# Optimization experiments

Measured on AMD Instinct MI355X. Metric: run time of the kernel, lower is better.

The kernel has to match this reference:

```python
import jax, jax.numpy as jnp
import numpy as np

N = 4608      # total nodes (48 graphs x 96 nodes)
B = 48
NPG = 96
D = 512       # vec_dim
XD = 16       # x_dim
E = N * 32    # GAT edges
L = 6         # GAT layers


def _w(k, shape, fan_in):
    return jax.random.normal(k, shape, jnp.float32) * (1.0 / np.sqrt(fan_in))


def setup_inputs() -> dict:
    key = jax.random.key(0)
    ks = jax.random.split(key, 24)
    x = jax.random.normal(ks[0], (N, XD), jnp.float32)
    xyz = jax.random.normal(ks[1], (N, 3), jnp.float32)
    edge_index = jax.random.randint(ks[2], (2, E), 0, N, dtype=jnp.int32)
    ptr = (jnp.arange(B + 1) * NPG).astype(jnp.int32)
    # complete graph with replacement per segment (torch.combinations order: i<=j)
    i, j = np.triu_indices(NPG)
    offs = (np.arange(B) * NPG)[:, None]
    cloud_edge_index = jnp.asarray(
        np.stack([(i[None, :] + offs).reshape(-1), (j[None, :] + offs).reshape(-1)]),
        jnp.int32)
    return {
        'x': x, 'edge_index': edge_index, 'ptr': ptr, 'xyz': xyz,
        'cloud_edge_index': cloud_edge_index,
        'x_proj_w': _w(ks[3], (XD, D), XD), 'x_proj_b': jnp.zeros((D,), jnp.float32),
        'gat_wl': _w(ks[4], (L, D, D), D), 'gat_bl': jnp.zeros((L, D), jnp.float32),
        'gat_wr': _w(ks[5], (L, D, D), D), 'gat_br': jnp.zeros((L, D), jnp.float32),
        'gat_att': _w(ks[6], (L, D), D), 'gat_bias': jnp.zeros((L, D), jnp.float32),
        'gat_ln_g': jnp.ones((L - 1, D), jnp.float32), 'gat_ln_b': jnp.zeros((L - 1, D), jnp.float32),
        'cg_xyz_w': _w(ks[7], (3, D), 3),
        'cg_bn_g': jnp.ones((D,), jnp.float32), 'cg_bn_b': jnp.zeros((D,), jnp.float32),
        'cg_lin1_w': _w(ks[8], (D, D), D), 'cg_lin1_b': jnp.zeros((D,), jnp.float32),
        'cg_ln_g': jnp.ones((D,), jnp.float32), 'cg_ln_b': jnp.zeros((D,), jnp.float32),
        'lin_w': _w(ks[9], (D, D), D), 'lin_b': jnp.zeros((D,), jnp.float32),
        'bn_g': jnp.ones((D,), jnp.float32), 'bn_b': jnp.zeros((D,), jnp.float32),
    }


def _batchnorm(t, g, b):
    mu = t.mean(0)
    v = ((t - mu) ** 2).mean(0)
    return (t - mu) / jnp.sqrt(v + 1e-5) * g + b


def _forward(x, edge_index, cloud_edge_index, x_proj_w, x_proj_b, gat_wl, gat_bl,
             gat_wr, gat_br, gat_att, gat_bias, gat_ln_g, gat_ln_b, cg_xyz_w,
             cg_bn_g, cg_bn_b, cg_lin1_w, cg_lin1_b, cg_ln_g, cg_ln_b,
             lin_w, lin_b, bn_g, bn_b, xyz):
    n = x.shape[0]
    h = x @ x_proj_w + x_proj_b  # [N, D]
    # ---- GATv2 stack (heads=1, self-loops added, eval mode: no dropout) ----
    loops = jnp.arange(n, dtype=edge_index.dtype)
    ei = jnp.concatenate([edge_index, jnp.stack([loops, loops])], axis=1)
    src, dst = ei[0], ei[1]
    xg = h
    for l in range(L):
        xl = xg @ gat_wl[l] + gat_bl[l]
        xr = xg @ gat_wr[l] + gat_br[l]
        e = jax.nn.leaky_relu(xl[src] + xr[dst], 0.2) @ gat_att[l]  # [E+N]
        m = jax.ops.segment_max(e, dst, num_segments=n)
        ew = jnp.exp(e - m[dst])
        den = jax.ops.segment_sum(ew, dst, num_segments=n)
        alpha = ew / den[dst]
        out = jax.ops.segment_sum(alpha[:, None] * xl[src], dst, num_segments=n) + gat_bias[l]
        if l < L - 1:
            # PyG LayerNorm, mode='graph', batch=None: normalize over all elements
            mu = out.mean()
            sd = jnp.sqrt(((out - mu) ** 2).mean())
            out = (out - mu) / (sd + 1e-5) * gat_ln_g[l] + gat_ln_b[l]
            out = jax.nn.relu(out)
        xg = out
    # ---- CloudGraph (complete graph gather-compute-scatter) ----
    a, b = cloud_edge_index[0], cloud_edge_index[1]
    rx = h[a] - h[b]          # [Ec, D]
    rz = xyz[a] - xyz[b]      # [Ec, 3]
    sq = (rz ** 2).sum(-1)
    dist = jnp.where(sq > 0, jnp.sqrt(jnp.where(sq > 0, sq, 1.0)), 0.0)
    w = jnp.exp(-dist)[:, None]
    p1 = jax.ops.segment_sum(jax.nn.relu((w * rx) @ cg_lin1_w + cg_lin1_b), a, num_segments=n)
    mu1 = p1.mean(-1, keepdims=True)
    v1 = ((p1 - mu1) ** 2).mean(-1, keepdims=True)
    ln1 = (p1 - mu1) / jnp.sqrt(v1 + 1e-5) * cg_ln_g + cg_ln_b
    p2 = jax.ops.segment_sum(jax.nn.relu(rz @ cg_xyz_w), a, num_segments=n)
    xc = h + ln1 + _batchnorm(p2, cg_bn_g, cg_bn_b)
    # ---- fuse + final norm ----
    return _batchnorm((h + xg + xc) @ lin_w + lin_b, bn_g, bn_b)


def reference(x, edge_index, ptr, xyz, cloud_edge_index, x_proj_w, x_proj_b,
              gat_wl, gat_bl, gat_wr, gat_br, gat_att, gat_bias, gat_ln_g,
              gat_ln_b, cg_xyz_w, cg_bn_g, cg_bn_b, cg_lin1_w, cg_lin1_b,
              cg_ln_g, cg_ln_b, lin_w, lin_b, bn_g, bn_b):
    return _forward(x, edge_index, cloud_edge_index, x_proj_w, x_proj_b, gat_wl,
                    gat_bl, gat_wr, gat_br, gat_att, gat_bias, gat_ln_g,
                    gat_ln_b, cg_xyz_w, cg_bn_g, cg_bn_b, cg_lin1_w, cg_lin1_b,
                    cg_ln_g, cg_ln_b, lin_w, lin_b, bn_g, bn_b, xyz)
```

## Files before the change

kernel.cpp:

```cpp
#include <hip/hip_runtime.h>
#include <hip/hip_bf16.h>

#define NN 4608
#define BG 48
#define NPG 96
#define DD 512
#define XDIM 16
#define EREAL 147456
#define NLAYER 6
#define NK 262144
#define TRIU 4656

typedef __hip_bfloat16 bf16;
typedef short short8 __attribute__((ext_vector_type(8)));
typedef short shortx4 __attribute__((ext_vector_type(4)));
typedef float f32x4 __attribute__((ext_vector_type(4)));
typedef float f32x2 __attribute__((ext_vector_type(2)));

__device__ __forceinline__ float s2f(short s) {
  return __uint_as_float(((unsigned int)(unsigned short)s) << 16);
}
__device__ __forceinline__ short f2bs(float f) {
  bf16 h = __float2bfloat16(f);
  short s;
  __builtin_memcpy(&s, &h, 2);
  return s;
}
__device__ __forceinline__ void f8x4(unsigned int w, float* o) {
  f32x2 a = __builtin_amdgcn_cvt_pk_f32_fp8(w, false);
  f32x2 b = __builtin_amdgcn_cvt_pk_f32_fp8(w, true);
  o[0] = a[0]; o[1] = a[1]; o[2] = b[0]; o[3] = b[1];
}
__device__ __forceinline__ void bf4(uint2 q, float* o) {
  o[0] = s2f((short)(q.x & 0xffff));
  o[1] = s2f((short)(q.x >> 16));
  o[2] = s2f((short)(q.y & 0xffff));
  o[3] = s2f((short)(q.y >> 16));
}

typedef const __attribute__((address_space(1))) unsigned int ga_u32;
typedef __attribute__((address_space(3))) unsigned int ls_u32;
__device__ __forceinline__ void gl16(const void* g, void* l) {
  __builtin_amdgcn_global_load_lds((ga_u32*)g, (ls_u32*)l, 16, 0, 0);
}

__global__ __launch_bounds__(256) void k_wt(const float* __restrict__ wl,
                                            const float* __restrict__ wr,
                                            const float* __restrict__ cg,
                                            const float* __restrict__ lin,
                                            bf16* __restrict__ Wt,
                                            int* __restrict__ counts,
                                            float* __restrict__ statsAll) {
  if (blockIdx.z == 0) {
    int id = (blockIdx.y * 16 + blockIdx.x) * 256 + threadIdx.x;
    if (id < NN) counts[id] = 0;
    if (id < 5 * 32) statsAll[id] = 0.f;
  }
  __shared__ float tile[32][33];
  int z = blockIdx.z;
  const float* src = (z < 6) ? wl + (size_t)z * NK
                   : (z < 12) ? wr + (size_t)(z - 6) * NK
                   : (z == 12) ? cg : lin;
  bf16* dst = Wt + (size_t)z * NK;
  int c = threadIdx.x & 31;
  int r0 = threadIdx.x >> 5;
  int bx = blockIdx.x * 32, by = blockIdx.y * 32;
#pragma unroll
  for (int i = 0; i < 4; i++) {
    int r = r0 + i * 8;
    tile[r][c] = src[(size_t)(by + r) * 512 + bx + c];
  }
  __syncthreads();
#pragma unroll
  for (int i = 0; i < 4; i++) {
    int r = r0 + i * 8;
    dst[(size_t)(bx + r) * 512 + by + c] = __float2bfloat16(tile[c][r]);
  }
}

__global__ void k_xproj(const float* __restrict__ x, const float* __restrict__ w,
                        const float* __restrict__ b, const int* __restrict__ ei,
                        const float* __restrict__ xyz,
                        bf16* __restrict__ h_bf, int* __restrict__ counts,
                        float* __restrict__ ep) {
  int i = blockIdx.x * blockDim.x + threadIdx.x;
  if (i >= NN * DD) return;
  if (i < EREAL) atomicAdd(&counts[ei[EREAL + i]], 1);
  if (i < NN * NPG) {
    int n = i / NPG, e = i - n * NPG;
    int p = n % NPG;
    if (e < NPG - p) {
      int g = n / NPG;
      int slot = g * TRIU + p * NPG - (p * (p - 1)) / 2 + e;
      int j = n + e;
      float dx = xyz[n * 3] - xyz[j * 3];
      float dy = xyz[n * 3 + 1] - xyz[j * 3 + 1];
      float dz = xyz[n * 3 + 2] - xyz[j * 3 + 2];
      float sq = dx * dx + dy * dy + dz * dz;
      float dist = (sq > 0.f) ? sqrtf(sq) : 0.f;
      float4 v;
      v.x = dx; v.y = dy; v.z = dz; v.w = __expf(-dist);
      *(float4*)&ep[(size_t)slot * 4] = v;
    }
  }
  int n = i >> 9, d = i & 511;
  float acc = b[d];
#pragma unroll
  for (int k = 0; k < XDIM; k++) acc += x[n * XDIM + k] * w[k * DD + d];
  h_bf[i] = __float2bfloat16(acc);
}

__global__ void k_scan(const int* __restrict__ counts, int* offsets, int* cursor) {
  __shared__ int part[256];
  int t = threadIdx.x;
  int base = t * 18;
  int s = 0;
#pragma unroll
  for (int i = 0; i < 18; i++) s += counts[base + i];
  part[t] = s;
  __syncthreads();
  for (int off = 1; off < 256; off <<= 1) {
    int v = part[t];
    int u = (t >= off) ? part[t - off] : 0;
    __syncthreads();
    part[t] = v + u;
    __syncthreads();
  }
  int run = t ? part[t - 1] : 0;
#pragma unroll
  for (int i = 0; i < 18; i++) {
    offsets[base + i] = run;
    cursor[base + i] = run;
    run += counts[base + i];
  }
  if (t == 0) offsets[NN] = EREAL;
}
__global__ void k_scatter(const int* __restrict__ ei, int* cursor, int* ssrc) {
  int e = blockIdx.x * blockDim.x + threadIdx.x;
  if (e < EREAL) {
    int s = ei[e], d = ei[EREAL + e];
    int pos = atomicAdd(&cursor[d], 1);
    ssrc[pos] = s;
  }
}

__global__ __launch_bounds__(256) void k_ln(bf16* __restrict__ xg,
                                            const float* __restrict__ stats,
                                            const float* __restrict__ g,
                                            const float* __restrict__ b,
                                            const float* __restrict__ p2,
                                            float* __restrict__ colsum,
                                            float* __restrict__ colsq) {
  if ((int)blockIdx.x >= 1152) {
    int r0 = (blockIdx.x - 1152) * 32;
    int c0 = threadIdx.x;
    float s0 = 0.f, q0 = 0.f, s1 = 0.f, q1 = 0.f;
    for (int r = r0; r < r0 + 32; ++r) {
      float v = p2[(size_t)r * 512 + c0];
      s0 += v; q0 += v * v;
      float w = p2[(size_t)r * 512 + c0 + 256];
      s1 += w; q1 += w * w;
    }
    atomicAdd(&colsum[c0], s0);
    atomicAdd(&colsq[c0], q0);
    atomicAdd(&colsum[c0 + 256], s1);
    atomicAdd(&colsq[c0 + 256], q1);
    return;
  }
  float s = 0.f, ss = 0.f;
#pragma unroll
  for (int i = 0; i < 16; i++) { s += stats[i]; ss += stats[16 + i]; }
  const float invM = 1.f / ((float)NN * (float)DD);
  float mu = s * invM;
  float var = ss * invM - mu * mu;
  float sd = sqrtf(fmaxf(var, 0.f));
  float inv = 1.f / (sd + 1e-5f);
  int i = blockIdx.x * 256 + threadIdx.x;
  int base = i * 8;
  int d0 = base & 511;
  short8 raw = *(const short8*)&xg[base];
  short8 pk;
#pragma unroll
  for (int k = 0; k < 8; k++) {
    float t = fmaxf((s2f(raw[k]) - mu) * inv * g[d0 + k] + b[d0 + k], 0.f);
    pk[k] = f2bs(t);
  }
  *(short8*)&xg[base] = pk;
}

__device__ __forceinline__ void gemm_tile(
    const bf16* __restrict__ Abf, const bf16* __restrict__ B,
    const float* __restrict__ bias,
    float* __restrict__ C, bf16* __restrict__ Cb, unsigned char* __restrict__ Cf8,
    float* __restrict__ csum, float* __restrict__ csq,
    int m0, int n0, bf16* As, bf16* Bs, float* cs, float* cq) {
  int tid = threadIdx.x;
  int lane = tid & 63, wid = tid >> 6;
  int mh = (wid >> 1) * 64, nh = (wid & 1) * 32;
  int l15 = lane & 15, quad = lane >> 4;
  int lr8 = lane >> 3, ls8 = lane & 7;
  int c16l = ls8 ^ lr8;
  int swzr = (l15 & 7) * 8;

  if (csum && tid < 64) { cs[tid] = 0.f; cq[tid] = 0.f; }

  const bf16* aSrc = Abf + (size_t)(m0 + wid * 32 + lr8) * 512 + c16l * 8;
  const bf16* bSrc = B   + (size_t)(n0 + wid * 16 + lr8) * 512 + c16l * 8;

#define STAGE(bi, kt) do {                                                   \
    gl16(aSrc + (kt) * 64,            As + (bi) * 8192 + (wid * 32     ) * 64); \
    gl16(aSrc + (kt) * 64 +  8 * 512, As + (bi) * 8192 + (wid * 32 +  8) * 64); \
    gl16(aSrc + (kt) * 64 + 16 * 512, As + (bi) * 8192 + (wid * 32 + 16) * 64); \
    gl16(aSrc + (kt) * 64 + 24 * 512, As + (bi) * 8192 + (wid * 32 + 24) * 64); \
    gl16(bSrc + (kt) * 64,            Bs + (bi) * 4096 + (wid * 16     ) * 64); \
    gl16(bSrc + (kt) * 64 +  8 * 512, Bs + (bi) * 4096 + (wid * 16 +  8) * 64); \
  } while (0)

  f32x4 acc[4][2];
#pragma unroll
  for (int mt = 0; mt < 4; mt++)
#pragma unroll
    for (int nt = 0; nt < 2; nt++) acc[mt][nt] = (f32x4)0.f;

  STAGE(0, 0);
  __syncthreads();

#pragma unroll
  for (int kt = 0; kt < 8; kt++) {
    const int cur = kt & 1;
    if (kt < 7) STAGE(cur ^ 1, kt + 1);
    short8 af[2][4], bfr[2][2];
#pragma unroll
    for (int kk = 0; kk < 2; kk++) {
#pragma unroll
      for (int mt = 0; mt < 4; mt++)
        af[kk][mt] = *(const short8*)&As[cur * 8192 + (mh + mt * 16 + l15) * 64 +
                                        (((kk * 4 + quad) * 8) ^ swzr)];
#pragma unroll
      for (int nt = 0; nt < 2; nt++)
        bfr[kk][nt] = *(const short8*)&Bs[cur * 4096 + (nh + nt * 16 + l15) * 64 +
                                         (((kk * 4 + quad) * 8) ^ swzr)];
    }
#pragma unroll
    for (int kk = 0; kk < 2; kk++)
#pragma unroll
      for (int mt = 0; mt < 4; mt++)
#pragma unroll
        for (int nt = 0; nt < 2; nt++)
          acc[mt][nt] = __builtin_amdgcn_mfma_f32_16x16x32_bf16(
              bfr[kk][nt], af[kk][mt], acc[mt][nt], 0, 0, 0);
    __syncthreads();
  }
#undef STAGE

  float colS[2][4] = {{0.f,0.f,0.f,0.f},{0.f,0.f,0.f,0.f}};
  float colQ[2][4] = {{0.f,0.f,0.f,0.f},{0.f,0.f,0.f,0.f}};
  float bv[2][4] = {{0.f,0.f,0.f,0.f},{0.f,0.f,0.f,0.f}};
#pragma unroll
  for (int nt = 0; nt < 2; nt++) {
    if (bias) {
      float4 b4 = *(const float4*)&bias[n0 + nh + nt * 16 + quad * 4];
      bv[nt][0] = b4.x; bv[nt][1] = b4.y; bv[nt][2] = b4.z; bv[nt][3] = b4.w;
    }
  }
#pragma unroll
  for (int mt = 0; mt < 4; mt++) {
    int row = m0 + mh + mt * 16 + l15;
#pragma unroll
    for (int nt = 0; nt < 2; nt++) {
      int col0 = n0 + nh + nt * 16 + quad * 4;
      float v[4];
#pragma unroll
      for (int r2 = 0; r2 < 4; r2++) {
        v[r2] = acc[mt][nt][r2] + bv[nt][r2];
        if (csum) { colS[nt][r2] += v[r2]; colQ[nt][r2] += v[r2] * v[r2]; }
      }
      if (C) {
        float4 o; o.x = v[0]; o.y = v[1]; o.z = v[2]; o.w = v[3];
        *(float4*)&C[(size_t)row * 512 + col0] = o;
      }
      if (Cb) {
        shortx4 o;
#pragma unroll
        for (int r2 = 0; r2 < 4; r2++) o[r2] = f2bs(v[r2]);
        *(shortx4*)&Cb[(size_t)row * 512 + col0] = o;
      }
      if (Cf8) {
        unsigned int u = __builtin_amdgcn_cvt_pk_fp8_f32(v[0], v[1], 0, false);
        u = __builtin_amdgcn_cvt_pk_fp8_f32(v[2], v[3], u, true);
        *(unsigned int*)&Cf8[(size_t)row * 512 + col0] = u;
      }
    }
  }
  if (csum) {
#pragma unroll
    for (int nt = 0; nt < 2; nt++)
#pragma unroll
      for (int r2 = 0; r2 < 4; r2++) {
        atomicAdd(&cs[nh + nt * 16 + quad * 4 + r2], colS[nt][r2]);
        atomicAdd(&cq[nh + nt * 16 + quad * 4 + r2], colQ[nt][r2]);
      }
    __syncthreads();
    if (tid < 64) {
      atomicAdd(&csum[n0 + tid], cs[tid]);
      atomicAdd(&csq[n0 + tid], cq[tid]);
    }
  }
}

__global__ __launch_bounds__(256) void k_gemm(
    const bf16* __restrict__ Abf,
    const bf16* __restrict__ B0, const bf16* __restrict__ B1,
    const float* __restrict__ bias0, const float* __restrict__ bias1,
    float* __restrict__ C0,
    bf16* __restrict__ Cb0, bf16* __restrict__ Cb1,
    unsigned char* __restrict__ Cf8_0,
    float* __restrict__ csum, float* __restrict__ csq, int nzl) {
  __shared__ __align__(16) bf16 As[2 * 128 * 64];
  __shared__ __align__(16) bf16 Bs[2 * 64 * 64];
  __shared__ float cs[64], cq[64];
  int cpx = gridDim.x >> 3;
  int wgid = (blockIdx.x & 7) * cpx + (blockIdx.x >> 3);
  int mi = wgid >> nzl;
  int r = wgid & ((1 << nzl) - 1);
  int z = r >> 3;
  int m0 = mi * 128, n0 = (r & 7) * 64;
  gemm_tile(Abf, z ? B1 : B0, z ? bias1 : bias0,
            z ? nullptr : C0, z ? Cb1 : Cb0, z ? nullptr : Cf8_0,
            csum, csq, m0, n0, As, Bs, cs, cq);
}

__global__ __launch_bounds__(256) void k_gemm_l0(
    const bf16* __restrict__ h_bf,
    const bf16* __restrict__ Bl, const bf16* __restrict__ Br,
    const float* __restrict__ biasl, const float* __restrict__ biasr,
    bf16* __restrict__ xr_bf, unsigned char* __restrict__ xl_f8,
    const bf16* __restrict__ Bg1, bf16* __restrict__ g1_bf,
    float* __restrict__ zptr) {
  __shared__ __align__(16) bf16 As[2 * 128 * 64];
  __shared__ __align__(16) bf16 Bs[2 * 64 * 64];
  int b = blockIdx.x;
  if (b < 576) {
    int cpx = 576 >> 3;
    int wgid = (b & 7) * cpx + (b >> 3);
    int mi = wgid >> 4;
    int r = wgid & 15;
    int z = r >> 3;
    int m0 = mi * 128, n0 = (r & 7) * 64;
    gemm_tile(h_bf, z ? Br : Bl, z ? biasr : biasl,
              nullptr, z ? xr_bf : nullptr, z ? nullptr : xl_f8,
              nullptr, nullptr, m0, n0, As, Bs, nullptr, nullptr);
  } else {
    int b2 = b - 576;
    if (b2 == 0) {
      for (int i = threadIdx.x; i < 1024; i += 256) zptr[i] = 0.f;
    }
    int cpx = 288 >> 3;
    int wgid = (b2 & 7) * cpx + (b2 >> 3);
    int mi = wgid >> 3;
    int r = wgid & 7;
    int m0 = mi * 128, n0 = r * 64;
    gemm_tile(h_bf, Bg1, nullptr, nullptr, g1_bf, nullptr,
              nullptr, nullptr, m0, n0, As, Bs, nullptr, nullptr);
  }
}

__device__ __forceinline__ void edge_block(
    const unsigned char* __restrict__ xl8, const bf16* __restrict__ xr,
    const float* __restrict__ att, const float* __restrict__ bias,
    const int* __restrict__ offs, const int* __restrict__ ssrc,
    bf16* __restrict__ out, float* __restrict__ statsOut,
    float* redS, float* redSS,
    const float* __restrict__ p1, const float* __restrict__ p2,
    const bf16* __restrict__ h_bf,
    const float* __restrict__ colsum, const float* __restrict__ colsq,
    const float* __restrict__ lng, const float* __restrict__ lnb,
    const float* __restrict__ bng, const float* __restrict__ bnb,
    bf16* __restrict__ s_bf, float* __restrict__ zptr) {
  if (zptr && blockIdx.x == 0) {
    for (int i = threadIdx.x; i < 1024; i += 256) zptr[i] = 0.f;
  }
  int wave = (blockIdx.x * blockDim.x + threadIdx.x) >> 6;
  int lane = threadIdx.x & 63;
  int wid = threadIdx.x >> 6;
  if (wave < NN) {
    int n = wave;
    int base = lane * 8;
    float xrv[8], attv[8], acc[8];
    short8 xr8 = *(const short8*)&xr[(size_t)n * 512 + base];
#pragma unroll
    for (int k = 0; k < 8; k++) {
      xrv[k] = s2f(xr8[k]);
      attv[k] = att[base + k];
    }
    float m0, lsum;
    {
      uint2 q = *(const uint2*)&xl8[(size_t)n * 512 + base];
      float xs[8];
      f8x4(q.x, xs);
      f8x4(q.y, xs + 4);
      float sc0 = 0.f;
#pragma unroll
      for (int k = 0; k < 8; k++) {
        acc[k] = xs[k];
        float t = xs[k] + xrv[k];
        t = (t > 0.f) ? t : 0.2f * t;
        sc0 += attv[k] * t;
      }
#pragma unroll
      for (int off = 32; off >= 1; off >>= 1) sc0 += __shfl_xor(sc0, off, 64);
      m0 = sc0;
      lsum = 1.f;
    }
    int e0 = offs[n], e1 = offs[n + 1];
    int e = e0;
    for (; e + 3 < e1; e += 4) {
      int s0 = ssrc[e], s1 = ssrc[e + 1], s2 = ssrc[e + 2], s3 = ssrc[e + 3];
      uint2 q0 = *(const uint2*)&xl8[(size_t)s0 * 512 + base];
      uint2 q1 = *(const uint2*)&xl8[(size_t)s1 * 512 + base];
      uint2 q2 = *(const uint2*)&xl8[(size_t)s2 * 512 + base];
      uint2 q3 = *(const uint2*)&xl8[(size_t)s3 * 512 + base];
      float x0[8], x1[8], x2[8], x3[8];
      f8x4(q0.x, x0); f8x4(q0.y, x0 + 4);
      f8x4(q1.x, x1); f8x4(q1.y, x1 + 4);
      f8x4(q2.x, x2); f8x4(q2.y, x2 + 4);
      f8x4(q3.x, x3); f8x4(q3.y, x3 + 4);
      float c0 = 0.f, c1 = 0.f, c2 = 0.f, c3 = 0.f;
#pragma unroll
      for (int k = 0; k < 8; k++) {
        float t0 = x0[k] + xrv[k]; t0 = (t0 > 0.f) ? t0 : 0.2f * t0; c0 += attv[k] * t0;
        float t1 = x1[k] + xrv[k]; t1 = (t1 > 0.f) ? t1 : 0.2f * t1; c1 += attv[k] * t1;
        float t2 = x2[k] + xrv[k]; t2 = (t2 > 0.f) ? t2 : 0.2f * t2; c2 += attv[k] * t2;
        float t3 = x3[k] + xrv[k]; t3 = (t3 > 0.f) ? t3 : 0.2f * t3; c3 += attv[k] * t3;
      }
#pragma unroll
      for (int off = 32; off >= 1; off >>= 1) {
        c0 += __shfl_xor(c0, off, 64);
        c1 += __shfl_xor(c1, off, 64);
        c2 += __shfl_xor(c2, off, 64);
        c3 += __shfl_xor(c3, off, 64);
      }
      float p0 = __expf(c0 - m0), pp1 = __expf(c1 - m0);
      float pp2 = __expf(c2 - m0), p3 = __expf(c3 - m0);
      lsum += p0 + pp1 + pp2 + p3;
#pragma unroll
      for (int k = 0; k < 8; k++)
        acc[k] += p0 * x0[k] + pp1 * x1[k] + pp2 * x2[k] + p3 * x3[k];
    }
    for (; e < e1; ++e) {
      int s0 = ssrc[e];
      uint2 q = *(const uint2*)&xl8[(size_t)s0 * 512 + base];
      float x0[8];
      f8x4(q.x, x0);
      f8x4(q.y, x0 + 4);
      float sc0 = 0.f;
#pragma unroll
      for (int k = 0; k < 8; k++) {
        float t0 = x0[k] + xrv[k];
        t0 = (t0 > 0.f) ? t0 : 0.2f * t0;
        sc0 += attv[k] * t0;
      }
#pragma unroll
      for (int off = 32; off >= 1; off >>= 1) sc0 += __shfl_xor(sc0, off, 64);
      float p0 = __expf(sc0 - m0);
      lsum += p0;
#pragma unroll
      for (int k = 0; k < 8; k++) acc[k] += p0 * x0[k];
    }
    float inv = 1.f / lsum;
    float o[8];
    float s = 0.f, ss = 0.f;
    short8 o8;
#pragma unroll
    for (int k = 0; k < 8; k++) {
      o[k] = acc[k] * inv + bias[base + k];
      s += o[k];
      ss += o[k] * o[k];
      o8[k] = f2bs(o[k]);
    }
    *(short8*)&out[(size_t)n * 512 + base] = o8;
    if (statsOut) {
#pragma unroll
      for (int off = 32; off >= 1; off >>= 1) {
        s += __shfl_xor(s, off, 64);
        ss += __shfl_xor(ss, off, 64);
      }
      if (lane == 0) { redS[wid] = s; redSS[wid] = ss; }
    }
    if (s_bf) {
      size_t rb = (size_t)n * 512 + base;
      float v[8];
      float sp = 0.f;
#pragma unroll
      for (int k = 0; k < 8; k++) {
        v[k] = p1[rb + k];
        sp += v[k];
      }
#pragma unroll
      for (int off = 32; off >= 1; off >>= 1) sp += __shfl_xor(sp, off, 64);
      float mu = sp * (1.f / 512.f);
      float ssp = 0.f;
#pragma unroll
      for (int k = 0; k < 8; k++) {
        float t = v[k] - mu;
        ssp += t * t;
      }
#pragma unroll
      for (int off = 32; off >= 1; off >>= 1) ssp += __shfl_xor(ssp, off, 64);
      float linv = 1.f / sqrtf(ssp * (1.f / 512.f) + 1e-5f);
      short8 hb = *(const short8*)&h_bf[rb];
      short8 e8;
#pragma unroll
      for (int k = 0; k < 8; k++) {
        int d = base + k;
        float ln1 = (v[k] - mu) * linv * lng[d] + lnb[d];
        float cmu = colsum[d] * (1.f / NN);
        float cvar = colsq[d] * (1.f / NN) - cmu * cmu;
        float cinv = 1.f / sqrtf(fmaxf(cvar, 0.f) + 1e-5f);
        float bnv = (p2[rb + k] - cmu) * cinv * bng[d] + bnb[d];
        float outv = 2.f * s2f(hb[k]) + s2f(o8[k]) + ln1 + bnv;
        e8[k] = f2bs(outv);
      }
      *(short8*)&s_bf[rb] = e8;
    }
  }
  if (statsOut) {
    __syncthreads();
    if (threadIdx.x == 0) {
      float a = redS[0] + redS[1] + redS[2] + redS[3];
      float b = redSS[0] + redSS[1] + redSS[2] + redSS[3];
      int slot = blockIdx.x & 15;
      atomicAdd(&statsOut[slot], a);
      atomicAdd(&statsOut[16 + slot], b);
    }
  }
}

__device__ __forceinline__ void cloud_wave(
    const bf16* __restrict__ g1, const float* __restrict__ ep,
    const float* __restrict__ lin1b, const float* __restrict__ w3,
    float* __restrict__ p1, float* __restrict__ p2, int w, int lane) {
  int qh = w & 1;
  int pi = w >> 1;
  int g = pi / 48, pp = pi % 48;
  int d0 = qh * 256 + lane * 4;
  float4 bb4 = *(const float4*)&lin1b[d0];
  float4 w04 = *(const float4*)&w3[d0];
  float4 w14 = *(const float4*)&w3[512 + d0];
  float4 w24 = *(const float4*)&w3[1024 + d0];
  float bb[4] = {bb4.x, bb4.y, bb4.z, bb4.w};
  float w0[4] = {w04.x, w04.y, w04.z, w04.w};
  float w1[4] = {w14.x, w14.y, w14.z, w14.w};
  float w2[4] = {w24.x, w24.y, w24.z, w24.w};

#pragma unroll
  for (int half = 0; half < 2; half++) {
    int p = half ? (NPG - 1 - pp) : pp;
    int n = g * NPG + p;
    int cnt = NPG - p;
    int slot0 = g * TRIU + p * NPG - (p * (p - 1)) / 2;
    const bf16* grow = &g1[(size_t)n * 512 + d0];
    float gi[4];
    { uint2 q = *(const uint2*)grow; bf4(q, gi); }
    float a1[4] = {0.f,0.f,0.f,0.f}, a2[4] = {0.f,0.f,0.f,0.f};
    float b1[4] = {0.f,0.f,0.f,0.f}, b2[4] = {0.f,0.f,0.f,0.f};
    int e = 0;
    for (; e + 3 < cnt; e += 4) {
      int sb = __builtin_amdgcn_readfirstlane(slot0 + e);
      float4 pa = *(const float4*)&ep[(size_t)sb * 4];
      float4 pb = *(const float4*)&ep[(size_t)(sb + 1) * 4];
      float4 pc = *(const float4*)&ep[(size_t)(sb + 2) * 4];
      float4 pd = *(const float4*)&ep[(size_t)(sb + 3) * 4];
      uint2 qa = *(const uint2*)&grow[(size_t)e * 512];
      uint2 qb = *(const uint2*)&grow[(size_t)(e + 1) * 512];
      uint2 qc = *(const uint2*)&grow[(size_t)(e + 2) * 512];
      uint2 qd = *(const uint2*)&grow[(size_t)(e + 3) * 512];
      float xa[4], xb[4], xc[4], xd[4];
      bf4(qa, xa); bf4(qb, xb); bf4(qc, xc); bf4(qd, xd);
      float t;
#pragma unroll
      for (int k = 0; k < 4; k++) {
        t = fmaf(pa.w, gi[k] - xa[k], bb[k]); a1[k] += fmaxf(t, 0.f);
        t = fmaf(pb.w, gi[k] - xb[k], bb[k]); b1[k] += fmaxf(t, 0.f);
        t = fmaf(pc.w, gi[k] - xc[k], bb[k]); a1[k] += fmaxf(t, 0.f);
        t = fmaf(pd.w, gi[k] - xd[k], bb[k]); b1[k] += fmaxf(t, 0.f);
        t = pa.x * w0[k] + pa.y * w1[k] + pa.z * w2[k]; a2[k] += fmaxf(t, 0.f);
        t = pb.x * w0[k] + pb.y * w1[k] + pb.z * w2[k]; b2[k] += fmaxf(t, 0.f);
        t = pc.x * w0[k] + pc.y * w1[k] + pc.z * w2[k]; a2[k] += fmaxf(t, 0.f);
        t = pd.x * w0[k] + pd.y * w1[k] + pd.z * w2[k]; b2[k] += fmaxf(t, 0.f);
      }
    }
    for (; e < cnt; ++e) {
      float4 pa = *(const float4*)&ep[(size_t)(slot0 + e) * 4];
      uint2 qa = *(const uint2*)&grow[(size_t)e * 512];
      float xa[4];
      bf4(qa, xa);
      float t;
#pragma unroll
      for (int k = 0; k < 4; k++) {
        t = fmaf(pa.w, gi[k] - xa[k], bb[k]); a1[k] += fmaxf(t, 0.f);
        t = pa.x * w0[k] + pa.y * w1[k] + pa.z * w2[k]; a2[k] += fmaxf(t, 0.f);
      }
    }
    float4 o1, o2;
    o1.x = a1[0] + b1[0]; o1.y = a1[1] + b1[1];
    o1.z = a1[2] + b1[2]; o1.w = a1[3] + b1[3];
    o2.x = a2[0] + b2[0]; o2.y = a2[1] + b2[1];
    o2.z = a2[2] + b2[2]; o2.w = a2[3] + b2[3];
    *(float4*)&p1[(size_t)n * 512 + d0] = o1;
    *(float4*)&p2[(size_t)n * 512 + d0] = o2;
  }
}

__global__ __launch_bounds__(256) void k_gat_edge(
    const unsigned char* __restrict__ xl8, const bf16* __restrict__ xr,
    const float* __restrict__ att, const float* __restrict__ bias,
    const int* __restrict__ offs, const int* __restrict__ ssrc,
    bf16* __restrict__ out, float* __restrict__ statsOut,
    const float* __restrict__ p1, const float* __restrict__ p2,
    const bf16* __restrict__ h_bf,
    const float* __restrict__ colsum, const float* __restrict__ colsq,
    const float* __restrict__ lng, const float* __restrict__ lnb,
    const float* __restrict__ bng, const float* __restrict__ bnb,
    bf16* __restrict__ s_bf, float* __restrict__ zptr) {
  __shared__ float redS[4], redSS[4];
  edge_block(xl8, xr, att, bias, offs, ssrc, out, statsOut, redS, redSS,
             p1, p2, h_bf, colsum, colsq, lng, lnb, bng, bnb, s_bf, zptr);
}

__global__ __launch_bounds__(256) void k_edge_cloud(
    const unsigned char* __restrict__ xl8, const bf16* __restrict__ xr,
    const float* __restrict__ att, const float* __restrict__ bias,
    const int* __restrict__ offs, const int* __restrict__ ssrc,
    bf16* __restrict__ out, float* __restrict__ statsOut,
    const bf16* __restrict__ g1, const float* __restrict__ ep,
    const float* __restrict__ lin1b, const float* __restrict__ w3,
    float* __restrict__ p1, float* __restrict__ p2) {
  __shared__ float redS[4], redSS[4];
  if ((int)blockIdx.x < 1152) {
    edge_block(xl8, xr, att, bias, offs, ssrc, out, statsOut, redS, redSS,
               nullptr, nullptr, nullptr, nullptr, nullptr, nullptr, nullptr,
               nullptr, nullptr, nullptr, nullptr);
  } else {
    int w = (blockIdx.x - 1152) * 4 + (threadIdx.x >> 6);
    cloud_wave(g1, ep, lin1b, w3, p1, p2, w, threadIdx.x & 63);
  }
}

__global__ void k_bn_out(const float* __restrict__ y, const float* __restrict__ colsum,
                         const float* __restrict__ colsq, const float* __restrict__ g,
                         const float* __restrict__ b, float* __restrict__ out) {
  int i = blockIdx.x * blockDim.x + threadIdx.x;
  if (i >= NN * DD) return;
  int d = i & 511;
  float mu = colsum[d] * (1.f / NN);
  float var = colsq[d] * (1.f / NN) - mu * mu;
  float inv = 1.f / sqrtf(fmaxf(var, 0.f) + 1e-5f);
  out[i] = (y[i] - mu) * inv * g[d] + b[d];
}

extern "C" void kernel_launch(void* const* d_in, const int* in_sizes, int n_in,
                              void* d_out, int out_size, void* d_ws, size_t ws_size,
                              hipStream_t stream) {
  const float* x = (const float*)d_in[0];
  const int* ei = (const int*)d_in[1];
  const float* xyz = (const float*)d_in[3];
  const float* x_proj_w = (const float*)d_in[5];
  const float* x_proj_b = (const float*)d_in[6];
  const float* gat_wl = (const float*)d_in[7];
  const float* gat_bl = (const float*)d_in[8];
  const float* gat_wr = (const float*)d_in[9];
  const float* gat_br = (const float*)d_in[10];
  const float* gat_att = (const float*)d_in[11];
  const float* gat_bias = (const float*)d_in[12];
  const float* gat_ln_g = (const float*)d_in[13];
  const float* gat_ln_b = (const float*)d_in[14];
  const float* cg_xyz_w = (const float*)d_in[15];
  const float* cg_bn_g = (const float*)d_in[16];
  const float* cg_bn_b = (const float*)d_in[17];
  const float* cg_lin1_w = (const float*)d_in[18];
  const float* cg_lin1_b = (const float*)d_in[19];
  const float* cg_ln_g = (const float*)d_in[20];
  const float* cg_ln_b = (const float*)d_in[21];
  const float* lin_w = (const float*)d_in[22];
  const float* lin_b = (const float*)d_in[23];
  const float* bn_g = (const float*)d_in[24];
  const float* bn_b = (const float*)d_in[25];

  const size_t ND = (size_t)NN * DD;
  char* w = (char*)d_ws;
  float* p1 = (float*)w;       w += ND * 4;
  float* p2 = (float*)w;       w += ND * 4;
  bf16* h_bf = (bf16*)w;       w += ND * 2;
  bf16* xg_bf = (bf16*)w;      w += ND * 2;
  bf16* g1_bf = (bf16*)w;      w += ND * 2;
  bf16* xr_bf = (bf16*)w;      w += ND * 2;
  unsigned char* xl_f8 = (unsigned char*)w; w += ND;
  bf16* Wt = (bf16*)w;         w += (size_t)14 * NK * 2;
  float* eparam = (float*)w;   w += (size_t)BG * TRIU * 16;
  int* counts = (int*)w;       w += NN * 4;
  int* offs = (int*)w;         w += (NN + 4) * 4;
  int* cursor = (int*)w;       w += NN * 4;
  int* ssrc = (int*)w;         w += EREAL * 4;
  float* statsAll = (float*)w; w += 5 * 32 * 4;
  float* colsum = (float*)w;   w += 512 * 4;
  float* colsq = (float*)w;    w += 512 * 4;
  float* colsum2 = (float*)w;  w += 512 * 4;
  float* colsq2 = (float*)w;   w += 512 * 4;
  float* y = p1;
  bf16* s_bf = h_bf;

  const int TPB = 256;
  const int ND_BLK = (int)((ND + TPB - 1) / TPB);

  k_wt<<<dim3(16, 16, 14), TPB, 0, stream>>>(gat_wl, gat_wr, cg_lin1_w, lin_w, Wt,
                                             counts, statsAll);
  k_xproj<<<ND_BLK, TPB, 0, stream>>>(x, x_proj_w, x_proj_b, ei, xyz, h_bf,
                                      counts, eparam);
  k_scan<<<1, 256, 0, stream>>>(counts, offs, cursor);
  k_scatter<<<(EREAL + TPB - 1) / TPB, TPB, 0, stream>>>(ei, cursor, ssrc);

  k_gemm_l0<<<864, TPB, 0, stream>>>(h_bf, Wt, Wt + (size_t)6 * NK,
                                     gat_bl, gat_br, xr_bf, xl_f8,
                                     Wt + (size_t)12 * NK, g1_bf, colsum);
  k_edge_cloud<<<1152 + 1152, TPB, 0, stream>>>(
      xl_f8, xr_bf, gat_att, gat_bias, offs, ssrc, xg_bf, statsAll,
      g1_bf, eparam, cg_lin1_b, cg_xyz_w, p1, p2);

  for (int l = 1; l < NLAYER; l++) {
    k_ln<<<(l == 1) ? 1296 : 1152, TPB, 0, stream>>>(
        xg_bf, statsAll + 32 * (l - 1),
        gat_ln_g + (size_t)(l - 1) * DD, gat_ln_b + (size_t)(l - 1) * DD,
        (l == 1) ? p2 : nullptr, colsum, colsq);
    k_gemm<<<576, TPB, 0, stream>>>(
        xg_bf, Wt + (size_t)l * NK, Wt + (size_t)(6 + l) * NK,
        gat_bl + l * DD, gat_br + l * DD, nullptr, nullptr, xr_bf,
        xl_f8, nullptr, nullptr, 4);
    float* sOut = (l < NLAYER - 1) ? statsAll + 32 * l : nullptr;
    bool last = (l == NLAYER - 1);
    k_gat_edge<<<NN / 4, TPB, 0, stream>>>(
        xl_f8, xr_bf, gat_att + l * DD, gat_bias + l * DD, offs, ssrc,
        xg_bf, sOut,
        last ? p1 : nullptr, last ? p2 : nullptr, last ? h_bf : nullptr,
        last ? colsum : nullptr, last ? colsq : nullptr,
        last ? cg_ln_g : nullptr, last ? cg_ln_b : nullptr,
        last ? cg_bn_g : nullptr, last ? cg_bn_b : nullptr,
        last ? s_bf : nullptr, last ? colsum2 : nullptr);
  }

  k_gemm<<<288, TPB, 0, stream>>>(
      s_bf, Wt + (size_t)13 * NK, Wt + (size_t)13 * NK, lin_b, lin_b,
      y, nullptr, nullptr, nullptr, colsum2, colsq2, 3);
  k_bn_out<<<ND_BLK, TPB, 0, stream>>>(y, colsum2, colsq2, bn_g, bn_b,
                                       (float*)d_out);
}
```

Before: 523.7 us.

## Split cloud edge sums into two halves, fuse scatter into GEMM, store g1 as fp32

Each cloud-conv wave's edge range is split in two. The two halves write separate partial buffers (p1a/p1b, p2a/p2b), which the LN and final-fuse consumers add back together; this doubles the cloud parallelism and evens out the triangular workload. The edge-scatter kernel is merged into the layer-0 GEMM launch as extra blocks, removing one launch. g1 is now stored in fp32 instead of bf16, which removes conversion work but doubles the read traffic for the cloud gathers and the workspace size.

```diff
diff --git a/kernel.cpp b/kernel.cpp
--- a/kernel.cpp
+++ b/kernel.cpp
@@ -30,12 +30,6 @@
   f32x2 a = __builtin_amdgcn_cvt_pk_f32_fp8(w, false);
   f32x2 b = __builtin_amdgcn_cvt_pk_f32_fp8(w, true);
   o[0] = a[0]; o[1] = a[1]; o[2] = b[0]; o[3] = b[1];
-}
-__device__ __forceinline__ void bf4(uint2 q, float* o) {
-  o[0] = s2f((short)(q.x & 0xffff));
-  o[1] = s2f((short)(q.x >> 16));
-  o[2] = s2f((short)(q.y & 0xffff));
-  o[3] = s2f((short)(q.y >> 16));
 }
 
 typedef const __attribute__((address_space(1))) unsigned int ga_u32;
@@ -135,20 +129,13 @@
   }
   if (t == 0) offsets[NN] = EREAL;
 }
-__global__ void k_scatter(const int* __restrict__ ei, int* cursor, int* ssrc) {
-  int e = blockIdx.x * blockDim.x + threadIdx.x;
-  if (e < EREAL) {
-    int s = ei[e], d = ei[EREAL + e];
-    int pos = atomicAdd(&cursor[d], 1);
-    ssrc[pos] = s;
-  }
-}
 
 __global__ __launch_bounds__(256) void k_ln(bf16* __restrict__ xg,
                                             const float* __restrict__ stats,
                                             const float* __restrict__ g,
                                             const float* __restrict__ b,
-                                            const float* __restrict__ p2,
+                                            const float* __restrict__ p2a,
+                                            const float* __restrict__ p2b,
                                             float* __restrict__ colsum,
                                             float* __restrict__ colsq) {
   if ((int)blockIdx.x >= 1152) {
@@ -156,9 +143,9 @@
     int c0 = threadIdx.x;
     float s0 = 0.f, q0 = 0.f, s1 = 0.f, q1 = 0.f;
     for (int r = r0; r < r0 + 32; ++r) {
-      float v = p2[(size_t)r * 512 + c0];
+      float v = p2a[(size_t)r * 512 + c0] + p2b[(size_t)r * 512 + c0];
       s0 += v; q0 += v * v;
-      float w = p2[(size_t)r * 512 + c0 + 256];
+      float w = p2a[(size_t)r * 512 + c0 + 256] + p2b[(size_t)r * 512 + c0 + 256];
       s1 += w; q1 += w * w;
     }
     atomicAdd(&colsum[c0], s0);
@@ -335,8 +322,9 @@
     const bf16* __restrict__ Bl, const bf16* __restrict__ Br,
     const float* __restrict__ biasl, const float* __restrict__ biasr,
     bf16* __restrict__ xr_bf, unsigned char* __restrict__ xl_f8,
-    const bf16* __restrict__ Bg1, bf16* __restrict__ g1_bf,
-    float* __restrict__ zptr) {
+    const bf16* __restrict__ Bg1, float* __restrict__ g1f,
+    float* __restrict__ zptr,
+    const int* __restrict__ ei, int* __restrict__ cursor, int* __restrict__ ssrc) {
   __shared__ __align__(16) bf16 As[2 * 128 * 64];
   __shared__ __align__(16) bf16 Bs[2 * 64 * 64];
   int b = blockIdx.x;
@@ -350,7 +338,7 @@
     gemm_tile(h_bf, z ? Br : Bl, z ? biasr : biasl,
               nullptr, z ? xr_bf : nullptr, z ? nullptr : xl_f8,
               nullptr, nullptr, m0, n0, As, Bs, nullptr, nullptr);
-  } else {
+  } else if (b < 864) {
     int b2 = b - 576;
     if (b2 == 0) {
       for (int i = threadIdx.x; i < 1024; i += 256) zptr[i] = 0.f;
@@ -360,8 +348,13 @@
     int mi = wgid >> 3;
     int r = wgid & 7;
     int m0 = mi * 128, n0 = r * 64;
-    gemm_tile(h_bf, Bg1, nullptr, nullptr, g1_bf, nullptr,
+    gemm_tile(h_bf, Bg1, nullptr, g1f, nullptr, nullptr,
               nullptr, nullptr, m0, n0, As, Bs, nullptr, nullptr);
+  } else {
+    int e = (b - 864) * 256 + threadIdx.x;
+    int s = ei[e], d = ei[EREAL + e];
+    int pos = atomicAdd(&cursor[d], 1);
+    ssrc[pos] = s;
   }
 }
 
@@ -371,7 +364,8 @@
     const int* __restrict__ offs, const int* __restrict__ ssrc,
     bf16* __restrict__ out, float* __restrict__ statsOut,
     float* redS, float* redSS,
-    const float* __restrict__ p1, const float* __restrict__ p2,
+    const float* __restrict__ p1a, const float* __restrict__ p1b,
+    const float* __restrict__ p2a, const float* __restrict__ p2b,
     const bf16* __restrict__ h_bf,
     const float* __restrict__ colsum, const float* __restrict__ colsq,
     const float* __restrict__ lng, const float* __restrict__ lnb,
@@ -493,7 +487,7 @@
       float sp = 0.f;
 #pragma unroll
       for (int k = 0; k < 8; k++) {
-        v[k] = p1[rb + k];
+        v[k] = p1a[rb + k] + p1b[rb + k];
         sp += v[k];
       }
 #pragma unroll
@@ -517,7 +511,8 @@
         float cmu = colsum[d] * (1.f / NN);
         float cvar = colsq[d] * (1.f / NN) - cmu * cmu;
         float cinv = 1.f / sqrtf(fmaxf(cvar, 0.f) + 1e-5f);
-        float bnv = (p2[rb + k] - cmu) * cinv * bng[d] + bnb[d];
+        float p2v = p2a[rb + k] + p2b[rb + k];
+        float bnv = (p2v - cmu) * cinv * bng[d] + bnb[d];
         float outv = 2.f * s2f(hb[k]) + s2f(o8[k]) + ln1 + bnv;
         e8[k] = f2bs(outv);
       }
@@ -537,11 +532,12 @@
 }
 
 __device__ __forceinline__ void cloud_wave(
-    const bf16* __restrict__ g1, const float* __restrict__ ep,
+    const float* __restrict__ g1f, const float* __restrict__ ep,
     const float* __restrict__ lin1b, const float* __restrict__ w3,
-    float* __restrict__ p1, float* __restrict__ p2, int w, int lane) {
+    float* __restrict__ p1c, float* __restrict__ p2c, int w, int lane) {
   int qh = w & 1;
-  int pi = w >> 1;
+  int c = (w >> 1) & 1;
+  int pi = w >> 2;
   int g = pi / 48, pp = pi % 48;
   int d0 = qh * 256 + lane * 4;
   float4 bb4 = *(const float4*)&lin1b[d0];
@@ -558,47 +554,51 @@
     int p = half ? (NPG - 1 - pp) : pp;
     int n = g * NPG + p;
     int cnt = NPG - p;
+    int h = cnt >> 1;
+    int eBeg = c ? h : 0;
+    int eEnd = c ? cnt : h;
     int slot0 = g * TRIU + p * NPG - (p * (p - 1)) / 2;
-    const bf16* grow = &g1[(size_t)n * 512 + d0];
-    float gi[4];
-    { uint2 q = *(const uint2*)grow; bf4(q, gi); }
+    const float* grow = &g1f[(size_t)n * 512 + d0];
+    float4 g4 = *(const float4*)grow;
+    float gi[4] = {g4.x, g4.y, g4.z, g4.w};
     float a1[4] = {0.f,0.f,0.f,0.f}, a2[4] = {0.f,0.f,0.f,0.f};
     float b1[4] = {0.f,0.f,0.f,0.f}, b2[4] = {0.f,0.f,0.f,0.f};
-    int e = 0;
-    for (; e + 3 < cnt; e += 4) {
+    int e = eBeg;
+    for (; e + 3 < eEnd; e += 4) {
       int sb = __builtin_amdgcn_readfirstlane(slot0 + e);
       float4 pa = *(const float4*)&ep[(size_t)sb * 4];
       float4 pb = *(const float4*)&ep[(size_t)(sb + 1) * 4];
       float4 pc = *(const float4*)&ep[(size_t)(sb + 2) * 4];
       float4 pd = *(const float4*)&ep[(size_t)(sb + 3) * 4];
-      uint2 qa = *(const uint2*)&grow[(size_t)e * 512];
-      uint2 qb = *(const uint2*)&grow[(size_t)(e + 1) * 512];
-      uint2 qc = *(const uint2*)&grow[(size_t)(e + 2) * 512];
-      uint2 qd = *(const uint2*)&grow[(size_t)(e + 3) * 512];
-      float xa[4], xb[4], xc[4], xd[4];
-      bf4(qa, xa); bf4(qb, xb); bf4(qc, xc); bf4(qd, xd);
+      float4 xa = *(const float4*)&grow[(size_t)e * 512];
+      float4 xb = *(const float4*)&grow[(size_t)(e + 1) * 512];
+      float4 xc = *(const float4*)&grow[(size_t)(e + 2) * 512];
+      float4 xd = *(const float4*)&grow[(size_t)(e + 3) * 512];
+      float xaf[4] = {xa.x, xa.y, xa.z, xa.w};
+      float xbf[4] = {xb.x, xb.y, xb.z, xb.w};
+      float xcf[4] = {xc.x, xc.y, xc.z, xc.w};
+      float xdf[4] = {xd.x, xd.y, xd.z, xd.w};
       float t;
 #pragma unroll
       for (int k = 0; k < 4; k++) {
-        t = fmaf(pa.w, gi[k] - xa[k], bb[k]); a1[k] += fmaxf(t, 0.f);
-        t = fmaf(pb.w, gi[k] - xb[k], bb[k]); b1[k] += fmaxf(t, 0.f);
-        t = fmaf(pc.w, gi[k] - xc[k], bb[k]); a1[k] += fmaxf(t, 0.f);
-        t = fmaf(pd.w, gi[k] - xd[k], bb[k]); b1[k] += fmaxf(t, 0.f);
+        t = fmaf(pa.w, gi[k] - xaf[k], bb[k]); a1[k] += fmaxf(t, 0.f);
+        t = fmaf(pb.w, gi[k] - xbf[k], bb[k]); b1[k] += fmaxf(t, 0.f);
+        t = fmaf(pc.w, gi[k] - xcf[k], bb[k]); a1[k] += fmaxf(t, 0.f);
+        t = fmaf(pd.w, gi[k] - xdf[k], bb[k]); b1[k] += fmaxf(t, 0.f);
         t = pa.x * w0[k] + pa.y * w1[k] + pa.z * w2[k]; a2[k] += fmaxf(t, 0.f);
         t = pb.x * w0[k] + pb.y * w1[k] + pb.z * w2[k]; b2[k] += fmaxf(t, 0.f);
         t = pc.x * w0[k] + pc.y * w1[k] + pc.z * w2[k]; a2[k] += fmaxf(t, 0.f);
         t = pd.x * w0[k] + pd.y * w1[k] + pd.z * w2[k]; b2[k] += fmaxf(t, 0.f);
       }
     }
-    for (; e < cnt; ++e) {
+    for (; e < eEnd; ++e) {
       float4 pa = *(const float4*)&ep[(size_t)(slot0 + e) * 4];
-      uint2 qa = *(const uint2*)&grow[(size_t)e * 512];
-      float xa[4];
-      bf4(qa, xa);
+      float4 xa = *(const float4*)&grow[(size_t)e * 512];
+      float xaf[4] = {xa.x, xa.y, xa.z, xa.w};
       float t;
 #pragma unroll
       for (int k = 0; k < 4; k++) {
-        t = fmaf(pa.w, gi[k] - xa[k], bb[k]); a1[k] += fmaxf(t, 0.f);
+        t = fmaf(pa.w, gi[k] - xaf[k], bb[k]); a1[k] += fmaxf(t, 0.f);
         t = pa.x * w0[k] + pa.y * w1[k] + pa.z * w2[k]; a2[k] += fmaxf(t, 0.f);
       }
     }
@@ -607,8 +607,8 @@
     o1.z = a1[2] + b1[2]; o1.w = a1[3] + b1[3];
     o2.x = a2[0] + b2[0]; o2.y = a2[1] + b2[1];
     o2.z = a2[2] + b2[2]; o2.w = a2[3] + b2[3];
-    *(float4*)&p1[(size_t)n * 512 + d0] = o1;
-    *(float4*)&p2[(size_t)n * 512 + d0] = o2;
+    *(float4*)&p1c[(size_t)n * 512 + d0] = o1;
+    *(float4*)&p2c[(size_t)n * 512 + d0] = o2;
   }
 }
 
@@ -617,7 +617,8 @@
     const float* __restrict__ att, const float* __restrict__ bias,
     const int* __restrict__ offs, const int* __restrict__ ssrc,
     bf16* __restrict__ out, float* __restrict__ statsOut,
-    const float* __restrict__ p1, const float* __restrict__ p2,
+    const float* __restrict__ p1a, const float* __restrict__ p1b,
+    const float* __restrict__ p2a, const float* __restrict__ p2b,
     const bf16* __restrict__ h_bf,
     const float* __restrict__ colsum, const float* __restrict__ colsq,
     const float* __restrict__ lng, const float* __restrict__ lnb,
@@ -625,7 +626,8 @@
     bf16* __restrict__ s_bf, float* __restrict__ zptr) {
   __shared__ float redS[4], redSS[4];
   edge_block(xl8, xr, att, bias, offs, ssrc, out, statsOut, redS, redSS,
-             p1, p2, h_bf, colsum, colsq, lng, lnb, bng, bnb, s_bf, zptr);
+             p1a, p1b, p2a, p2b, h_bf, colsum, colsq, lng, lnb, bng, bnb,
+             s_bf, zptr);
 }
 
 __global__ __launch_bounds__(256) void k_edge_cloud(
@@ -633,17 +635,20 @@
     const float* __restrict__ att, const float* __restrict__ bias,
     const int* __restrict__ offs, const int* __restrict__ ssrc,
     bf16* __restrict__ out, float* __restrict__ statsOut,
-    const bf16* __restrict__ g1, const float* __restrict__ ep,
+    const float* __restrict__ g1f, const float* __restrict__ ep,
     const float* __restrict__ lin1b, const float* __restrict__ w3,
-    float* __restrict__ p1, float* __restrict__ p2) {
+    float* __restrict__ p1a, float* __restrict__ p1b,
+    float* __restrict__ p2a, float* __restrict__ p2b) {
   __shared__ float redS[4], redSS[4];
   if ((int)blockIdx.x < 1152) {
     edge_block(xl8, xr, att, bias, offs, ssrc, out, statsOut, redS, redSS,
                nullptr, nullptr, nullptr, nullptr, nullptr, nullptr, nullptr,
-               nullptr, nullptr, nullptr, nullptr);
+               nullptr, nullptr, nullptr, nullptr, nullptr, nullptr);
   } else {
     int w = (blockIdx.x - 1152) * 4 + (threadIdx.x >> 6);
-    cloud_wave(g1, ep, lin1b, w3, p1, p2, w, threadIdx.x & 63);
+    int c = (w >> 1) & 1;
+    cloud_wave(g1f, ep, lin1b, w3, c ? p1b : p1a, c ? p2b : p2a,
+               w, threadIdx.x & 63);
   }
 }
 
@@ -689,11 +694,13 @@
 
   const size_t ND = (size_t)NN * DD;
   char* w = (char*)d_ws;
-  float* p1 = (float*)w;       w += ND * 4;
-  float* p2 = (float*)w;       w += ND * 4;
+  float* p1a = (float*)w;      w += ND * 4;
+  float* p2a = (float*)w;      w += ND * 4;
+  float* p1b = (float*)w;      w += ND * 4;
+  float* p2b = (float*)w;      w += ND * 4;
+  float* g1f = (float*)w;      w += ND * 4;
   bf16* h_bf = (bf16*)w;       w += ND * 2;
   bf16* xg_bf = (bf16*)w;      w += ND * 2;
-  bf16* g1_bf = (bf16*)w;      w += ND * 2;
   bf16* xr_bf = (bf16*)w;      w += ND * 2;
   unsigned char* xl_f8 = (unsigned char*)w; w += ND;
   bf16* Wt = (bf16*)w;         w += (size_t)14 * NK * 2;
@@ -707,7 +714,7 @@
   float* colsq = (float*)w;    w += 512 * 4;
   float* colsum2 = (float*)w;  w += 512 * 4;
   float* colsq2 = (float*)w;   w += 512 * 4;
-  float* y = p1;
+  float* y = p1a;
   bf16* s_bf = h_bf;
 
   const int TPB = 256;
@@ -718,20 +725,20 @@
   k_xproj<<<ND_BLK, TPB, 0, stream>>>(x, x_proj_w, x_proj_b, ei, xyz, h_bf,
                                       counts, eparam);
   k_scan<<<1, 256, 0, stream>>>(counts, offs, cursor);
-  k_scatter<<<(EREAL + TPB - 1) / TPB, TPB, 0, stream>>>(ei, cursor, ssrc);
-
-  k_gemm_l0<<<864, TPB, 0, stream>>>(h_bf, Wt, Wt + (size_t)6 * NK,
-                                     gat_bl, gat_br, xr_bf, xl_f8,
-                                     Wt + (size_t)12 * NK, g1_bf, colsum);
-  k_edge_cloud<<<1152 + 1152, TPB, 0, stream>>>(
+
+  k_gemm_l0<<<1440, TPB, 0, stream>>>(h_bf, Wt, Wt + (size_t)6 * NK,
+                                      gat_bl, gat_br, xr_bf, xl_f8,
+                                      Wt + (size_t)12 * NK, g1f, colsum,
+                                      ei, cursor, ssrc);
+  k_edge_cloud<<<1152 + 2304, TPB, 0, stream>>>(
       xl_f8, xr_bf, gat_att, gat_bias, offs, ssrc, xg_bf, statsAll,
-      g1_bf, eparam, cg_lin1_b, cg_xyz_w, p1, p2);
+      g1f, eparam, cg_lin1_b, cg_xyz_w, p1a, p1b, p2a, p2b);
 
   for (int l = 1; l < NLAYER; l++) {
     k_ln<<<(l == 1) ? 1296 : 1152, TPB, 0, stream>>>(
         xg_bf, statsAll + 32 * (l - 1),
         gat_ln_g + (size_t)(l - 1) * DD, gat_ln_b + (size_t)(l - 1) * DD,
-        (l == 1) ? p2 : nullptr, colsum, colsq);
+        (l == 1) ? p2a : nullptr, (l == 1) ? p2b : nullptr, colsum, colsq);
     k_gemm<<<576, TPB, 0, stream>>>(
         xg_bf, Wt + (size_t)l * NK, Wt + (size_t)(6 + l) * NK,
         gat_bl + l * DD, gat_br + l * DD, nullptr, nullptr, xr_bf,
@@ -741,7 +748,9 @@
     k_gat_edge<<<NN / 4, TPB, 0, stream>>>(
         xl_f8, xr_bf, gat_att + l * DD, gat_bias + l * DD, offs, ssrc,
         xg_bf, sOut,
-        last ? p1 : nullptr, last ? p2 : nullptr, last ? h_bf : nullptr,
+        last ? p1a : nullptr, last ? p1b : nullptr,
+        last ? p2a : nullptr, last ? p2b : nullptr,
+        last ? h_bf : nullptr,
         last ? colsum : nullptr, last ? colsq : nullptr,
         last ? cg_ln_g : nullptr, last ? cg_ln_b : nullptr,
         last ? cg_bn_g : nullptr, last ? cg_bn_b : nullptr,
```

Result: faster. 511.9 us (-2.3%).
